# Optimization experiments

Measured on AMD Instinct MI355X. Metric: run time of the kernel, lower is better.

Reference implementation:

```python
import jax, jax.numpy as jnp
import numpy as np

N_NODES = 100000
NUM_REL = 2


def rgcn_conv(x, src, dst, etype, W, root, bias):
    """PyG-style RGCNConv: per-relation mean aggregation + root transform + bias.
    x: [N, in], W: [R, in, out], root: [in, out], bias: [out].
    """
    R = W.shape[0]
    N = x.shape[0]
    # Pre-transform nodes by every relation weight: [R, N, out]
    xr = jnp.einsum('ni,rio->rno', x, W)
    msgs = xr[etype, src]  # [E, out] gather per-edge, relation-typed
    seg_id = dst * R + etype  # combined (node, relation) segment id
    summed = jax.ops.segment_sum(msgs, seg_id, num_segments=N * R)
    cnt = jax.ops.segment_sum(jnp.ones(etype.shape, x.dtype), seg_id, num_segments=N * R)
    summed = summed.reshape(N, R, -1)
    cnt = cnt.reshape(N, R, 1)
    agg = (summed / jnp.maximum(cnt, 1.0)).sum(axis=1)  # sum over relations of per-relation means
    return agg + x @ root + bias


def setup_inputs() -> dict:
    key = jax.random.key(0)
    ks = jax.random.split(key, 9)
    d = 128
    E = 800000
    sc = 1.0 / np.sqrt(d)
    return {
        'x': jax.random.normal(ks[0], (N_NODES, d), jnp.float32),
        'edge_index_a': jax.random.randint(ks[1], (2, E), 0, N_NODES, jnp.int64),
        'edge_index_b': jax.random.randint(ks[2], (2, E), 0, N_NODES, jnp.int64),
        'W1': jax.random.normal(ks[3], (NUM_REL, d, d), jnp.float32) * sc,
        'root1': jax.random.normal(ks[4], (d, d), jnp.float32) * sc,
        'b1': jnp.zeros((d,), jnp.float32),
        'W2': jax.random.normal(ks[5], (NUM_REL, d, d), jnp.float32) * sc,
        'root2': jax.random.normal(ks[6], (d, d), jnp.float32) * sc,
        'b2': jnp.zeros((d,), jnp.float32),
    }


def reference(x, edge_index_a, edge_index_b, W1, root1, b1, W2, root2, b2):
    # Concatenate per-relation edge lists + build edge_type ids (a->0, b->1)
    edge_index = jnp.concatenate([edge_index_a, edge_index_b], axis=1)
    etype = jnp.concatenate([
        jnp.zeros((edge_index_a.shape[1],), jnp.int32),
        jnp.ones((edge_index_b.shape[1],), jnp.int32),
    ])
    src, dst = edge_index[0], edge_index[1]
    h = rgcn_conv(x, src, dst, etype, W1, root1, b1)
    h = jax.nn.relu(h)
    out = rgcn_conv(h, src, dst, etype, W2, root2, b2)
    return out
```

## Files before the change

kernel.cpp:

```cpp
#include <hip/hip_runtime.h>
#include <hip/hip_bf16.h>


typedef __attribute__((ext_vector_type(8))) short bf16x8;
typedef __attribute__((ext_vector_type(4))) float f32x4;
typedef unsigned short ushort_t;
typedef unsigned int uint_t;

#define BSHIFT 9
#define SEGB (1 << (BSHIFT + 1))
#define NBMAX 256
#define CH_PER_THREAD 16
#define CHUNK (256 * CH_PER_THREAD)

#define GBM 256
#define KCH 192
#define LDBB 400

__device__ __forceinline__ float b2fu(uint_t u) {
  union { uint_t u; float f; } v;
  v.u = u << 16;
  return v.f;
}
__device__ __forceinline__ ushort_t f2b(float f) {
  union { float f; uint_t u; } v;
  v.f = f;
  uint_t u = v.u;
  return (ushort_t)((u + 0x7FFFu + ((u >> 16) & 1u)) >> 16);
}

__global__ __launch_bounds__(384) void btbuild(
    const float* __restrict__ W, const float* __restrict__ root,
    ushort_t* __restrict__ Bt) {
  int c = blockIdx.x;
  int k = threadIdx.x;
  float v = (k < 256) ? W[(size_t)k * 128 + c] : root[(size_t)(k - 256) * 128 + c];
  Bt[(size_t)c * 384 + k] = f2b(v);
}

__global__ __launch_bounds__(256) void xstage(
    const float* __restrict__ x, ushort_t* __restrict__ aggbuf, int N) {
  int idx = blockIdx.x * blockDim.x + threadIdx.x;
  int n = idx >> 6, lane = idx & 63;
  if (n >= N) return;
  float2 v = *(const float2*)(x + (size_t)n * 128 + lane * 2);
  uint_t pk = (uint_t)f2b(v.x) | ((uint_t)f2b(v.y) << 16);
  *(uint_t*)(aggbuf + (size_t)n * 384 + 256 + lane * 2) = pk;
}

__global__ __launch_bounds__(256) void bucket_hist(
    const int* __restrict__ ea, const int* __restrict__ eb,
    int E, int NB, int* __restrict__ bucket_cnt) {
  __shared__ int h[NBMAX];
  for (int i = threadIdx.x; i < NB; i += 256) h[i] = 0;
  __syncthreads();
  int tbase = blockIdx.x * CHUNK + threadIdx.x;
  int total = 2 * E;
#pragma unroll
  for (int j = 0; j < CH_PER_THREAD; ++j) {
    int i = tbase + j * 256;
    if (i < total) {
      int dst = (i < E) ? ea[E + i] : eb[i];
      atomicAdd(&h[dst >> BSHIFT], 1);
    }
  }
  __syncthreads();
  for (int i = threadIdx.x; i < NB; i += 256)
    if (h[i]) atomicAdd(&bucket_cnt[i], h[i]);
}

__global__ __launch_bounds__(256) void bucket_scan(
    const int* __restrict__ bucket_cnt, int* __restrict__ bucket_base,
    int* __restrict__ bucket_cursor, int NB) {
  __shared__ int sdata[256];
  int v = (threadIdx.x < NB) ? bucket_cnt[threadIdx.x] : 0;
  sdata[threadIdx.x] = v;
  __syncthreads();
  for (int off = 1; off < 256; off <<= 1) {
    int t = (threadIdx.x >= (unsigned)off) ? sdata[threadIdx.x - off] : 0;
    __syncthreads();
    sdata[threadIdx.x] += t;
    __syncthreads();
  }
  if (threadIdx.x < NB) {
    int e = sdata[threadIdx.x] - v;
    bucket_base[threadIdx.x] = e;
    bucket_cursor[threadIdx.x] = e;
  }
}

__global__ __launch_bounds__(256) void bucket_bin(
    const int* __restrict__ ea, const int* __restrict__ eb,
    int E, int NB, int* __restrict__ bucket_cursor,
    uint2* __restrict__ staging) {
  __shared__ int h[NBMAX];
  __shared__ int bbase[NBMAX];
  for (int i = threadIdx.x; i < NB; i += 256) h[i] = 0;
  __syncthreads();
  int tbase = blockIdx.x * CHUNK + threadIdx.x;
  int total = 2 * E;
  uint2 val[CH_PER_THREAD];
#pragma unroll
  for (int j = 0; j < CH_PER_THREAD; ++j) {
    int i = tbase + j * 256;
    if (i < total) {
      int src, dst, rel;
      if (i < E) { src = ea[i];     dst = ea[E + i]; rel = 0; }
      else       { src = eb[i - E]; dst = eb[i];     rel = 1; }
      val[j].x = (uint_t)src;
      val[j].y = (uint_t)(dst * 2 + rel);
      atomicAdd(&h[dst >> BSHIFT], 1);
    } else {
      val[j].y = 0xffffffffu;
    }
  }
  __syncthreads();
  for (int i = threadIdx.x; i < NB; i += 256) {
    int c = h[i];
    bbase[i] = c ? atomicAdd(&bucket_cursor[i], c) : 0;
    h[i] = 0;
  }
  __syncthreads();
#pragma unroll
  for (int j = 0; j < CH_PER_THREAD; ++j) {
    if (val[j].y != 0xffffffffu) {
      int bkt = (int)(val[j].y >> (BSHIFT + 1));
      int r = atomicAdd(&h[bkt], 1);
      staging[(size_t)bbase[bkt] + r] = val[j];
    }
  }
}

__global__ __launch_bounds__(256) void bucket_build(
    const uint2* __restrict__ staging,
    const int* __restrict__ bucket_base, const int* __restrict__ bucket_cnt,
    int* __restrict__ csr, int* __restrict__ offs, int* __restrict__ ends,
    int nseg) {
  __shared__ int scnt[SEGB];
  __shared__ int sexcl[SEGB];
  __shared__ int sdata[256];
  int b = blockIdx.x;
  int base = bucket_base[b];
  int ne = bucket_cnt[b];
  int seg0 = b << (BSHIFT + 1);
  int t = threadIdx.x;
  for (int i = t; i < SEGB; i += 256) scnt[i] = 0;
  __syncthreads();
  const uint2* st = staging + base;
  for (int i = t; i < ne; i += 256) {
    int seg = (int)st[i].y - seg0;
    atomicAdd(&scnt[seg], 1);
  }
  __syncthreads();
  int c0 = scnt[t * 4 + 0], c1 = scnt[t * 4 + 1];
  int c2 = scnt[t * 4 + 2], c3 = scnt[t * 4 + 3];
  int s = c0 + c1 + c2 + c3;
  sdata[t] = s;
  __syncthreads();
  for (int off = 1; off < 256; off <<= 1) {
    int tmp = (t >= (unsigned)off) ? sdata[t - off] : 0;
    __syncthreads();
    sdata[t] += tmp;
    __syncthreads();
  }
  int excl = sdata[t] - s;
  int e0 = excl, e1 = excl + c0, e2 = e1 + c1, e3 = e2 + c2;
  sexcl[t * 4 + 0] = e0;
  sexcl[t * 4 + 1] = e1;
  sexcl[t * 4 + 2] = e2;
  sexcl[t * 4 + 3] = e3;
  {
    int g = seg0 + t * 4;
    if (g + 0 < nseg) { offs[g + 0] = base + e0; ends[g + 0] = base + e0 + c0; }
    if (g + 1 < nseg) { offs[g + 1] = base + e1; ends[g + 1] = base + e1 + c1; }
    if (g + 2 < nseg) { offs[g + 2] = base + e2; ends[g + 2] = base + e2 + c2; }
    if (g + 3 < nseg) { offs[g + 3] = base + e3; ends[g + 3] = base + e3 + c3; }
  }
  scnt[t * 4 + 0] = 0;
  scnt[t * 4 + 1] = 0;
  scnt[t * 4 + 2] = 0;
  scnt[t * 4 + 3] = 0;
  __syncthreads();
  for (int i = t; i < ne; i += 256) {
    uint2 v = st[i];
    int seg = (int)v.y - seg0;
    int r = atomicAdd(&scnt[seg], 1);
    csr[base + sexcl[seg] + r] = (int)v.x;
  }
}

__device__ __forceinline__ void accum8(float* acc, uint4 v) {
  acc[0] += b2fu(v.x); acc[1] += b2fu(v.x >> 16);
  acc[2] += b2fu(v.y); acc[3] += b2fu(v.y >> 16);
  acc[4] += b2fu(v.z); acc[5] += b2fu(v.z >> 16);
  acc[6] += b2fu(v.w); acc[7] += b2fu(v.w >> 16);
}

__global__ __launch_bounds__(256) void agg_kernel(
    const ushort_t* __restrict__ xb,
    const int* __restrict__ csr,
    const int* __restrict__ offs, const int* __restrict__ ends,
    ushort_t* __restrict__ agg, int nseg) {
  int wid = (blockIdx.x * blockDim.x + threadIdx.x) >> 6;
  if (wid >= nseg) return;
  int lane = threadIdx.x & 63;
  int q = lane >> 4;
  int t = lane & 15;
  int beg = offs[wid], end = ends[wid];

  float acc[8];
#pragma unroll
  for (int j = 0; j < 8; ++j) acc[j] = 0.f;

  int e = beg + q;
  for (; e + 4 < end; e += 8) {
    int s0 = csr[e];
    int s1 = csr[e + 4];
    uint4 v0 = *(const uint4*)(xb + (size_t)s0 * 384 + 256 + t * 8);
    uint4 v1 = *(const uint4*)(xb + (size_t)s1 * 384 + 256 + t * 8);
    accum8(acc, v0);
    accum8(acc, v1);
  }
  if (e < end) {
    int s0 = csr[e];
    uint4 v0 = *(const uint4*)(xb + (size_t)s0 * 384 + 256 + t * 8);
    accum8(acc, v0);
  }

#pragma unroll
  for (int j = 0; j < 8; ++j) {
    acc[j] += __shfl_xor(acc[j], 16);
    acc[j] += __shfl_xor(acc[j], 32);
  }

  int c = end - beg;
  float inv = 1.0f / (float)(c > 1 ? c : 1);
  if (q == 0) {
    uint4 o;
    o.x = (uint_t)f2b(acc[0] * inv) | ((uint_t)f2b(acc[1] * inv) << 16);
    o.y = (uint_t)f2b(acc[2] * inv) | ((uint_t)f2b(acc[3] * inv) << 16);
    o.z = (uint_t)f2b(acc[4] * inv) | ((uint_t)f2b(acc[5] * inv) << 16);
    o.w = (uint_t)f2b(acc[6] * inv) | ((uint_t)f2b(acc[7] * inv) << 16);
    int n = wid >> 1, r = wid & 1;
    *(uint4*)(agg + (size_t)n * 384 + r * 128 + t * 8) = o;
  }
}


__device__ __forceinline__ void do_mfma32(
    const ushort_t* Bs, f32x4 (&acc)[4][8], const bf16x8 (&a)[4],
    int ks, int lrow, int kg) {
  bf16x8 b[8];
#pragma unroll
  for (int c = 0; c < 8; ++c)
    b[c] = *(const bf16x8*)((const char*)Bs + (c * 16 + lrow) * LDBB +
                            (ks * 4 + kg) * 16);
#pragma unroll
  for (int r = 0; r < 4; ++r)
#pragma unroll
    for (int c = 0; c < 8; ++c)
      acc[r][c] = __builtin_amdgcn_mfma_f32_16x16x32_bf16(a[r], b[c], acc[r][c], 0, 0, 0);
}

template <int MODE>
__global__ __launch_bounds__(256, 2) void mfma_gemm(
    const ushort_t* __restrict__ A,
    const ushort_t* __restrict__ Bt,
    const float* __restrict__ bias,
    float* __restrict__ outf,
    ushort_t* __restrict__ outb,
    int M) {
  __shared__ __align__(16) ushort_t Bs[128 * (LDBB / 2)];
  const int tid = threadIdx.x;
  const int lane = tid & 63;
  const int wave = tid >> 6;
  const int lrow = lane & 15;
  const int kg = lane >> 4;
  const int rowbase = blockIdx.x * GBM + wave * 64;

  f32x4 acc[4][8];
#pragma unroll
  for (int r = 0; r < 4; ++r)
#pragma unroll
    for (int c = 0; c < 8; ++c) acc[r][c] = (f32x4){0.f, 0.f, 0.f, 0.f};

  for (int ch = 0; ch < 2; ++ch) {
#pragma unroll
    for (int j = 0; j < 12; ++j) {
      int flat = tid + j * 256;
      int col = flat / 24;
      int q = flat - col * 24;
      uint4 v = *(const uint4*)(Bt + (size_t)col * 384 + ch * KCH + q * 8);
      *(uint4*)((char*)Bs + col * LDBB + q * 16) = v;
    }
    __syncthreads();

    const ushort_t* ab = A + (size_t)ch * KCH + kg * 8;
    bf16x8 aA[4], aB[4];
#pragma unroll
    for (int r = 0; r < 4; ++r)
      aA[r] = *(const bf16x8*)(ab + (size_t)(rowbase + r * 16 + lrow) * 384);
#pragma unroll
    for (int ks2 = 0; ks2 < 3; ++ks2) {
      {
        const int ks = ks2 * 2;
#pragma unroll
        for (int r = 0; r < 4; ++r)
          aB[r] = *(const bf16x8*)(ab + (size_t)(rowbase + r * 16 + lrow) * 384 +
                                   (ks + 1) * 32);
        do_mfma32(Bs, acc, aA, ks, lrow, kg);
      }
      {
        const int ks = ks2 * 2 + 1;
        if (ks < 5) {
#pragma unroll
          for (int r = 0; r < 4; ++r)
            aA[r] = *(const bf16x8*)(ab + (size_t)(rowbase + r * 16 + lrow) * 384 +
                                     (ks + 1) * 32);
        }
        do_mfma32(Bs, acc, aB, ks, lrow, kg);
      }
    }
    __syncthreads();
  }

#pragma unroll
  for (int c = 0; c < 8; ++c) {
    int col = c * 16 + lrow;
    float bv = bias[col];
#pragma unroll
    for (int r = 0; r < 4; ++r) {
      int r0 = rowbase + r * 16 + kg * 4;
#pragma unroll
      for (int j = 0; j < 4; ++j) {
        int row = r0 + j;
        if (row < M) {
          float v = acc[r][c][j] + bv;
          if (MODE == 1) {
            v = fmaxf(v, 0.f);
            outb[(size_t)row * 384 + 256 + col] = f2b(v);
          } else {
            outf[(size_t)row * 128 + col] = v;
          }
        }
      }
    }
  }
}

extern "C" void kernel_launch(void* const* d_in, const int* in_sizes, int n_in,
                              void* d_out, int out_size, void* d_ws, size_t ws_size,
                              hipStream_t stream) {
  const float* x     = (const float*)d_in[0];
  const int*   ea    = (const int*)d_in[1];
  const int*   eb    = (const int*)d_in[2];
  const float* W1    = (const float*)d_in[3];
  const float* root1 = (const float*)d_in[4];
  const float* b1    = (const float*)d_in[5];
  const float* W2    = (const float*)d_in[6];
  const float* root2 = (const float*)d_in[7];
  const float* b2    = (const float*)d_in[8];
  float* out = (float*)d_out;

  const int N = in_sizes[0] / 128;
  const int E = in_sizes[1] / 2;
  const int nseg = N * 2;
  const int Mblk = (N + GBM - 1) / GBM;
  const int Mpad = Mblk * GBM;
  const int NB = ((N - 1) >> BSHIFT) + 1;
  const int nchunk = (2 * E + CHUNK - 1) / CHUNK;

  char* p = (char*)d_ws;
  ushort_t* aggbuf1 = (ushort_t*)p;  p += (size_t)Mpad * 384 * sizeof(ushort_t);
  ushort_t* aggbuf2 = (ushort_t*)p;  p += (size_t)Mpad * 384 * sizeof(ushort_t);
  ushort_t* Bt1 = (ushort_t*)p;      p += (size_t)128 * 384 * sizeof(ushort_t);
  ushort_t* Bt2 = (ushort_t*)p;      p += (size_t)128 * 384 * sizeof(ushort_t);
  int* csr = (int*)p;                p += (size_t)2 * E * sizeof(int);
  int* offs = (int*)p;               p += (size_t)nseg * sizeof(int);
  int* ends = (int*)p;               p += (size_t)nseg * sizeof(int);
  int* bucket_cnt = (int*)p;         p += NBMAX * sizeof(int);
  int* bucket_base = (int*)p;        p += NBMAX * sizeof(int);
  int* bucket_cursor = (int*)p;      p += NBMAX * sizeof(int);
  uint2* staging = (uint2*)aggbuf2;

  hipMemsetAsync(bucket_cnt, 0, NBMAX * sizeof(int), stream);

  btbuild<<<128, 384, 0, stream>>>(W1, root1, Bt1);
  btbuild<<<128, 384, 0, stream>>>(W2, root2, Bt2);
  xstage<<<(N * 64 + 255) / 256, 256, 0, stream>>>(x, aggbuf1, N);

  bucket_hist<<<nchunk, 256, 0, stream>>>(ea, eb, E, NB, bucket_cnt);
  bucket_scan<<<1, 256, 0, stream>>>(bucket_cnt, bucket_base, bucket_cursor, NB);
  bucket_bin<<<nchunk, 256, 0, stream>>>(ea, eb, E, NB, bucket_cursor, staging);
  bucket_build<<<NB, 256, 0, stream>>>(staging, bucket_base, bucket_cnt,
                                       csr, offs, ends, nseg);

  const int agg_blocks = (nseg + 3) / 4;

  agg_kernel<<<agg_blocks, 256, 0, stream>>>(aggbuf1, csr, offs, ends, aggbuf1, nseg);
  mfma_gemm<1><<<Mblk, 256, 0, stream>>>(aggbuf1, Bt1, b1, nullptr, aggbuf2, N);

  agg_kernel<<<agg_blocks, 256, 0, stream>>>(aggbuf2, csr, offs, ends, aggbuf2, nseg);
  mfma_gemm<0><<<Mblk, 256, 0, stream>>>(aggbuf2, Bt2, b2, out, nullptr, N);
}
```

Measured before the change: 340.2 us.

## Fuse prep kernels, fold bucket scan into consumers, double-buffer GEMM B tiles

Merges weight transposition, x staging and the bucket histogram into one multi-role launch. The single-block scan kernel is removed and each bin/build block recomputes the bucket prefix locally, with the cursor now zeroed by an enlarged memset. The GEMM B-tile staging changes from two 192-wide K chunks to three 128-wide chunks in a double-buffered LDS with register prefetch, so the global loads of the next chunk overlap the current MFMAs. This cuts launch count and serialization at the cost of redundant scans per block and more LDS per GEMM block.

```diff
diff --git a/kernel.cpp b/kernel.cpp
--- a/kernel.cpp
+++ b/kernel.cpp
@@ -14,8 +14,8 @@
 #define CHUNK (256 * CH_PER_THREAD)
 
 #define GBM 256
-#define KCH 192
-#define LDBB 400
+#define KCH 128
+#define LDBE 136
 
 __device__ __forceinline__ float b2fu(uint_t u) {
   union { uint_t u; float f; } v;
@@ -29,75 +29,76 @@
   return (ushort_t)((u + 0x7FFFu + ((u >> 16) & 1u)) >> 16);
 }
 
-__global__ __launch_bounds__(384) void btbuild(
-    const float* __restrict__ W, const float* __restrict__ root,
-    ushort_t* __restrict__ Bt) {
-  int c = blockIdx.x;
-  int k = threadIdx.x;
-  float v = (k < 256) ? W[(size_t)k * 128 + c] : root[(size_t)(k - 256) * 128 + c];
-  Bt[(size_t)c * 384 + k] = f2b(v);
-}
-
-__global__ __launch_bounds__(256) void xstage(
-    const float* __restrict__ x, ushort_t* __restrict__ aggbuf, int N) {
-  int idx = blockIdx.x * blockDim.x + threadIdx.x;
-  int n = idx >> 6, lane = idx & 63;
-  if (n >= N) return;
-  float2 v = *(const float2*)(x + (size_t)n * 128 + lane * 2);
-  uint_t pk = (uint_t)f2b(v.x) | ((uint_t)f2b(v.y) << 16);
-  *(uint_t*)(aggbuf + (size_t)n * 384 + 256 + lane * 2) = pk;
-}
-
-__global__ __launch_bounds__(256) void bucket_hist(
-    const int* __restrict__ ea, const int* __restrict__ eb,
-    int E, int NB, int* __restrict__ bucket_cnt) {
+__global__ __launch_bounds__(256) void prep(
+    const float* __restrict__ W1, const float* __restrict__ root1,
+    const float* __restrict__ W2, const float* __restrict__ root2,
+    ushort_t* __restrict__ Bt1, ushort_t* __restrict__ Bt2,
+    const float* __restrict__ x, ushort_t* __restrict__ aggbuf1, int N,
+    const int* __restrict__ ea, const int* __restrict__ eb, int E, int NB,
+    int* __restrict__ bucket_cnt, int XSB) {
   __shared__ int h[NBMAX];
-  for (int i = threadIdx.x; i < NB; i += 256) h[i] = 0;
-  __syncthreads();
-  int tbase = blockIdx.x * CHUNK + threadIdx.x;
-  int total = 2 * E;
-#pragma unroll
-  for (int j = 0; j < CH_PER_THREAD; ++j) {
-    int i = tbase + j * 256;
-    if (i < total) {
-      int dst = (i < E) ? ea[E + i] : eb[i];
-      atomicAdd(&h[dst >> BSHIFT], 1);
-    }
-  }
-  __syncthreads();
-  for (int i = threadIdx.x; i < NB; i += 256)
-    if (h[i]) atomicAdd(&bucket_cnt[i], h[i]);
-}
-
-__global__ __launch_bounds__(256) void bucket_scan(
-    const int* __restrict__ bucket_cnt, int* __restrict__ bucket_base,
-    int* __restrict__ bucket_cursor, int NB) {
-  __shared__ int sdata[256];
-  int v = (threadIdx.x < NB) ? bucket_cnt[threadIdx.x] : 0;
-  sdata[threadIdx.x] = v;
-  __syncthreads();
-  for (int off = 1; off < 256; off <<= 1) {
-    int t = (threadIdx.x >= (unsigned)off) ? sdata[threadIdx.x - off] : 0;
-    __syncthreads();
-    sdata[threadIdx.x] += t;
-    __syncthreads();
-  }
-  if (threadIdx.x < NB) {
-    int e = sdata[threadIdx.x] - v;
-    bucket_base[threadIdx.x] = e;
-    bucket_cursor[threadIdx.x] = e;
+  int b = blockIdx.x;
+  if (b < 384) {
+    int flat = b * 256 + threadIdx.x;
+    int which = flat >= 49152;
+    int idx = flat - which * 49152;
+    int c = idx / 384;
+    int k = idx - c * 384;
+    const float* W = which ? W2 : W1;
+    const float* root = which ? root2 : root1;
+    ushort_t* Bt = which ? Bt2 : Bt1;
+    float v = (k < 256) ? W[(size_t)k * 128 + c] : root[(size_t)(k - 256) * 128 + c];
+    Bt[(size_t)c * 384 + k] = f2b(v);
+  } else if (b < 384 + XSB) {
+    int idx = (b - 384) * 256 + threadIdx.x;
+    int n = idx >> 6, lane = idx & 63;
+    if (n < N) {
+      float2 v = *(const float2*)(x + (size_t)n * 128 + lane * 2);
+      uint_t pk = (uint_t)f2b(v.x) | ((uint_t)f2b(v.y) << 16);
+      *(uint_t*)(aggbuf1 + (size_t)n * 384 + 256 + lane * 2) = pk;
+    }
+  } else {
+    for (int i = threadIdx.x; i < NB; i += 256) h[i] = 0;
+    __syncthreads();
+    int tbase = (b - 384 - XSB) * CHUNK + threadIdx.x;
+    int total = 2 * E;
+#pragma unroll
+    for (int j = 0; j < CH_PER_THREAD; ++j) {
+      int i = tbase + j * 256;
+      if (i < total) {
+        int dst = (i < E) ? ea[E + i] : eb[i];
+        atomicAdd(&h[dst >> BSHIFT], 1);
+      }
+    }
+    __syncthreads();
+    for (int i = threadIdx.x; i < NB; i += 256)
+      if (h[i]) atomicAdd(&bucket_cnt[i], h[i]);
   }
 }
 
 __global__ __launch_bounds__(256) void bucket_bin(
     const int* __restrict__ ea, const int* __restrict__ eb,
-    int E, int NB, int* __restrict__ bucket_cursor,
-    uint2* __restrict__ staging) {
+    int E, int NB, const int* __restrict__ bucket_cnt,
+    int* __restrict__ bucket_cursor, uint2* __restrict__ staging) {
   __shared__ int h[NBMAX];
   __shared__ int bbase[NBMAX];
-  for (int i = threadIdx.x; i < NB; i += 256) h[i] = 0;
-  __syncthreads();
-  int tbase = blockIdx.x * CHUNK + threadIdx.x;
+  __shared__ int gbase[NBMAX];
+  __shared__ int sdata[256];
+  int t = threadIdx.x;
+  int v = (t < NB) ? bucket_cnt[t] : 0;
+  sdata[t] = v;
+  __syncthreads();
+  for (int off = 1; off < 256; off <<= 1) {
+    int tmp = (t >= off) ? sdata[t - off] : 0;
+    __syncthreads();
+    sdata[t] += tmp;
+    __syncthreads();
+  }
+  if (t < NB) gbase[t] = sdata[t] - v;
+  for (int i = t; i < NB; i += 256) h[i] = 0;
+  __syncthreads();
+
+  int tbase = blockIdx.x * CHUNK + t;
   int total = 2 * E;
   uint2 val[CH_PER_THREAD];
 #pragma unroll
@@ -115,9 +116,9 @@
     }
   }
   __syncthreads();
-  for (int i = threadIdx.x; i < NB; i += 256) {
+  for (int i = t; i < NB; i += 256) {
     int c = h[i];
-    bbase[i] = c ? atomicAdd(&bucket_cursor[i], c) : 0;
+    bbase[i] = c ? gbase[i] + atomicAdd(&bucket_cursor[i], c) : 0;
     h[i] = 0;
   }
   __syncthreads();
@@ -132,18 +133,28 @@
 }
 
 __global__ __launch_bounds__(256) void bucket_build(
-    const uint2* __restrict__ staging,
-    const int* __restrict__ bucket_base, const int* __restrict__ bucket_cnt,
-    int* __restrict__ csr, int* __restrict__ offs, int* __restrict__ ends,
-    int nseg) {
+    const uint2* __restrict__ staging, const int* __restrict__ bucket_cnt,
+    int NB, int* __restrict__ csr, int* __restrict__ offs,
+    int* __restrict__ ends, int nseg) {
   __shared__ int scnt[SEGB];
   __shared__ int sexcl[SEGB];
   __shared__ int sdata[256];
   int b = blockIdx.x;
-  int base = bucket_base[b];
+  int t = threadIdx.x;
+  int v = (t < NB) ? bucket_cnt[t] : 0;
+  sdata[t] = v;
+  __syncthreads();
+  for (int off = 1; off < 256; off <<= 1) {
+    int tmp = (t >= off) ? sdata[t - off] : 0;
+    __syncthreads();
+    sdata[t] += tmp;
+    __syncthreads();
+  }
+  int base = sdata[b] - bucket_cnt[b];
   int ne = bucket_cnt[b];
   int seg0 = b << (BSHIFT + 1);
-  int t = threadIdx.x;
+  __syncthreads();
+
   for (int i = t; i < SEGB; i += 256) scnt[i] = 0;
   __syncthreads();
   const uint2* st = staging + base;
@@ -158,7 +169,7 @@
   sdata[t] = s;
   __syncthreads();
   for (int off = 1; off < 256; off <<= 1) {
-    int tmp = (t >= (unsigned)off) ? sdata[t - off] : 0;
+    int tmp = (t >= off) ? sdata[t - off] : 0;
     __syncthreads();
     sdata[t] += tmp;
     __syncthreads();
@@ -182,10 +193,10 @@
   scnt[t * 4 + 3] = 0;
   __syncthreads();
   for (int i = t; i < ne; i += 256) {
-    uint2 v = st[i];
-    int seg = (int)v.y - seg0;
+    uint2 vrec = st[i];
+    int seg = (int)vrec.y - seg0;
     int r = atomicAdd(&scnt[seg], 1);
-    csr[base + sexcl[seg] + r] = (int)v.x;
+    csr[base + sexcl[seg] + r] = (int)vrec.x;
   }
 }
 
@@ -248,12 +259,12 @@
 
 
 __device__ __forceinline__ void do_mfma32(
-    const ushort_t* Bs, f32x4 (&acc)[4][8], const bf16x8 (&a)[4],
+    const char* bs, f32x4 (&acc)[4][8], const bf16x8 (&a)[4],
     int ks, int lrow, int kg) {
   bf16x8 b[8];
 #pragma unroll
   for (int c = 0; c < 8; ++c)
-    b[c] = *(const bf16x8*)((const char*)Bs + (c * 16 + lrow) * LDBB +
+    b[c] = *(const bf16x8*)(bs + (c * 16 + lrow) * (LDBE * 2) +
                             (ks * 4 + kg) * 16);
 #pragma unroll
   for (int r = 0; r < 4; ++r)
@@ -270,7 +281,7 @@
     float* __restrict__ outf,
     ushort_t* __restrict__ outb,
     int M) {
-  __shared__ __align__(16) ushort_t Bs[128 * (LDBB / 2)];
+  __shared__ __align__(16) ushort_t Bs[2][128 * LDBE];
   const int tid = threadIdx.x;
   const int lane = tid & 63;
   const int wave = tid >> 6;
@@ -284,44 +295,65 @@
 #pragma unroll
     for (int c = 0; c < 8; ++c) acc[r][c] = (f32x4){0.f, 0.f, 0.f, 0.f};
 
-  for (int ch = 0; ch < 2; ++ch) {
-#pragma unroll
-    for (int j = 0; j < 12; ++j) {
-      int flat = tid + j * 256;
-      int col = flat / 24;
-      int q = flat - col * 24;
-      uint4 v = *(const uint4*)(Bt + (size_t)col * 384 + ch * KCH + q * 8);
-      *(uint4*)((char*)Bs + col * LDBB + q * 16) = v;
-    }
-    __syncthreads();
-
+  uint4 stg[8];
+#pragma unroll
+  for (int j = 0; j < 8; ++j) {
+    int flat = tid + j * 256;
+    int col = flat >> 4;
+    int q = flat & 15;
+    stg[j] = *(const uint4*)(Bt + (size_t)col * 384 + q * 8);
+  }
+#pragma unroll
+  for (int j = 0; j < 8; ++j) {
+    int flat = tid + j * 256;
+    int col = flat >> 4;
+    int q = flat & 15;
+    *(uint4*)((char*)&Bs[0][0] + col * (LDBE * 2) + q * 16) = stg[j];
+  }
+  __syncthreads();
+
+  int cur = 0;
+  for (int ch = 0; ch < 3; ++ch) {
+    if (ch < 2) {
+#pragma unroll
+      for (int j = 0; j < 8; ++j) {
+        int flat = tid + j * 256;
+        int col = flat >> 4;
+        int q = flat & 15;
+        stg[j] = *(const uint4*)(Bt + (size_t)col * 384 + (ch + 1) * KCH + q * 8);
+      }
+    }
     const ushort_t* ab = A + (size_t)ch * KCH + kg * 8;
+    const char* bsbase = (const char*)&Bs[0][0] + cur * (128 * LDBE * 2);
     bf16x8 aA[4], aB[4];
 #pragma unroll
     for (int r = 0; r < 4; ++r)
       aA[r] = *(const bf16x8*)(ab + (size_t)(rowbase + r * 16 + lrow) * 384);
 #pragma unroll
-    for (int ks2 = 0; ks2 < 3; ++ks2) {
-      {
-        const int ks = ks2 * 2;
-#pragma unroll
-        for (int r = 0; r < 4; ++r)
-          aB[r] = *(const bf16x8*)(ab + (size_t)(rowbase + r * 16 + lrow) * 384 +
-                                   (ks + 1) * 32);
-        do_mfma32(Bs, acc, aA, ks, lrow, kg);
+    for (int r = 0; r < 4; ++r)
+      aB[r] = *(const bf16x8*)(ab + (size_t)(rowbase + r * 16 + lrow) * 384 + 32);
+    do_mfma32(bsbase, acc, aA, 0, lrow, kg);
+#pragma unroll
+    for (int r = 0; r < 4; ++r)
+      aA[r] = *(const bf16x8*)(ab + (size_t)(rowbase + r * 16 + lrow) * 384 + 64);
+    do_mfma32(bsbase, acc, aB, 1, lrow, kg);
+#pragma unroll
+    for (int r = 0; r < 4; ++r)
+      aB[r] = *(const bf16x8*)(ab + (size_t)(rowbase + r * 16 + lrow) * 384 + 96);
+    do_mfma32(bsbase, acc, aA, 2, lrow, kg);
+    do_mfma32(bsbase, acc, aB, 3, lrow, kg);
+    if (ch < 2) {
+#pragma unroll
+      for (int j = 0; j < 8; ++j) {
+        int flat = tid + j * 256;
+        int col = flat >> 4;
+        int q = flat & 15;
+        *(uint4*)((char*)&Bs[0][0] + (cur ^ 1) * (128 * LDBE * 2) +
+                  col * (LDBE * 2) + q * 16) = stg[j];
       }
-      {
-        const int ks = ks2 * 2 + 1;
-        if (ks < 5) {
-#pragma unroll
-          for (int r = 0; r < 4; ++r)
-            aA[r] = *(const bf16x8*)(ab + (size_t)(rowbase + r * 16 + lrow) * 384 +
-                                     (ks + 1) * 32);
-        }
-        do_mfma32(Bs, acc, aB, ks, lrow, kg);
-      }
-    }
-    __syncthreads();
+      __syncthreads();
+      cur ^= 1;
+    }
   }
 
 #pragma unroll
@@ -369,6 +401,7 @@
   const int Mpad = Mblk * GBM;
   const int NB = ((N - 1) >> BSHIFT) + 1;
   const int nchunk = (2 * E + CHUNK - 1) / CHUNK;
+  const int XSB = (N * 64 + 255) / 256;
 
   char* p = (char*)d_ws;
   ushort_t* aggbuf1 = (ushort_t*)p;  p += (size_t)Mpad * 384 * sizeof(ushort_t);
@@ -379,20 +412,18 @@
   int* offs = (int*)p;               p += (size_t)nseg * sizeof(int);
   int* ends = (int*)p;               p += (size_t)nseg * sizeof(int);
   int* bucket_cnt = (int*)p;         p += NBMAX * sizeof(int);
-  int* bucket_base = (int*)p;        p += NBMAX * sizeof(int);
   int* bucket_cursor = (int*)p;      p += NBMAX * sizeof(int);
   uint2* staging = (uint2*)aggbuf2;
 
-  hipMemsetAsync(bucket_cnt, 0, NBMAX * sizeof(int), stream);
-
-  btbuild<<<128, 384, 0, stream>>>(W1, root1, Bt1);
-  btbuild<<<128, 384, 0, stream>>>(W2, root2, Bt2);
-  xstage<<<(N * 64 + 255) / 256, 256, 0, stream>>>(x, aggbuf1, N);
-
-  bucket_hist<<<nchunk, 256, 0, stream>>>(ea, eb, E, NB, bucket_cnt);
-  bucket_scan<<<1, 256, 0, stream>>>(bucket_cnt, bucket_base, bucket_cursor, NB);
-  bucket_bin<<<nchunk, 256, 0, stream>>>(ea, eb, E, NB, bucket_cursor, staging);
-  bucket_build<<<NB, 256, 0, stream>>>(staging, bucket_base, bucket_cnt,
+  hipMemsetAsync(bucket_cnt, 0, 2 * NBMAX * sizeof(int), stream);
+
+  prep<<<384 + XSB + nchunk, 256, 0, stream>>>(
+      W1, root1, W2, root2, Bt1, Bt2, x, aggbuf1, N,
+      ea, eb, E, NB, bucket_cnt, XSB);
+
+  bucket_bin<<<nchunk, 256, 0, stream>>>(ea, eb, E, NB, bucket_cnt,
+                                         bucket_cursor, staging);
+  bucket_build<<<NB, 256, 0, stream>>>(staging, bucket_cnt, NB,
                                        csr, offs, ends, nseg);
 
   const int agg_blocks = (nseg + 3) / 4;
```

After: 342.4 us. No clear change (+0.6%).
